# Performance work log

Hardware: AMD Instinct MI355X
Metric: run time of the kernel (lower is better)

Reference implementation:

```python
import jax, jax.numpy as jnp
import numpy as np

B, L, E, C = 64, 1024, 320, 32
H = int(E * 1.5)  # hidden_dim = 480
LAYER_NUM = 7
EPS = 1e-5


def setup_inputs() -> dict:
    key = jax.random.key(0)
    ks = jax.random.split(key, 12)
    rn = lambda k, shape: jax.random.normal(k, shape, jnp.float32) * 0.02
    return {
        "x": jax.random.normal(ks[0], (B, L, E), jnp.float32),
        "snr": jnp.array([10.0], jnp.float32),
        # final LayerNorm params
        "norm_w": jnp.ones((E,), jnp.float32),
        "norm_b": jnp.zeros((E,), jnp.float32),
        "sm0_w": rn(ks[1], (H, E)), "sm0_b": jnp.zeros((H,), jnp.float32),
        "sm_mid_w": rn(ks[2], (LAYER_NUM - 1, H, H)), "sm_mid_b": jnp.zeros((LAYER_NUM - 1, H), jnp.float32),
        "sm_last_w": rn(ks[3], (E, H)), "sm_last_b": jnp.zeros((E,), jnp.float32),
        # bm_list: 7 AdaptiveModulators, each Linear(1,H)->ReLU->Linear(H,H)->ReLU->Linear(H,H)->Sigmoid
        "bm_w1": rn(ks[4], (LAYER_NUM, H, 1)), "bm_b1": jnp.zeros((LAYER_NUM, H), jnp.float32),
        "bm_w2": rn(ks[5], (LAYER_NUM, H, H)), "bm_b2": jnp.zeros((LAYER_NUM, H), jnp.float32),
        "bm_w3": rn(ks[6], (LAYER_NUM, H, H)), "bm_b3": jnp.zeros((LAYER_NUM, H), jnp.float32),
        # head_list: Linear(E, C)
        "head_w": rn(ks[7], (C, E)), "head_b": jnp.zeros((C,), jnp.float32),
    }


def reference(x, snr, norm_w, norm_b, sm0_w, sm0_b, sm_mid_w, sm_mid_b,
              sm_last_w, sm_last_b, bm_w1, bm_b1, bm_w2, bm_b2, bm_w3, bm_b3,
              head_w, head_b):
    # Final encoder LayerNorm (torch default: biased var, eps=1e-5)
    mu = jnp.mean(x, axis=-1, keepdims=True)
    var = jnp.var(x, axis=-1, keepdims=True)
    xn = (x - mu) / jnp.sqrt(var + EPS) * norm_w + norm_b  # (B, L, E)

    b = x.shape[0]
    snr_batch = jnp.broadcast_to(snr.reshape(1, -1), (b, 1))  # (B, 1)

    # SA modulation chain (x is detached for the modulator input)
    temp = jax.lax.stop_gradient(xn) @ sm0_w.T + sm0_b  # (B, L, H)
    for i in range(LAYER_NUM):
        if i > 0:
            temp = temp @ sm_mid_w[i - 1].T + sm_mid_b[i - 1]
        h = jax.nn.relu(snr_batch @ bm_w1[i].T + bm_b1[i])      # (B, H)
        h = jax.nn.relu(h @ bm_w2[i].T + bm_b2[i])
        bm = jax.nn.sigmoid(h @ bm_w3[i].T + bm_b3[i])          # (B, H)
        temp = temp * bm[:, None, :]

    mod_val = jax.nn.sigmoid(temp @ sm_last_w.T + sm_last_b)    # (B, L, E)
    xg = xn * mod_val
    return xg @ head_w.T + head_b                               # (B, L, C)
```

## Files before the change

kernel.cpp:

```cpp
#include <hip/hip_runtime.h>

#define E_ 320
#define C_ 32
#define H_ 480
#define NL 7
#define EPS_ 1e-5f

typedef unsigned short u16;
typedef __attribute__((ext_vector_type(8))) short short8;
typedef __attribute__((ext_vector_type(4))) float f32x4;

__device__ __forceinline__ float bsf(u16 u) { return __uint_as_float(((unsigned)u) << 16); }
__device__ __forceinline__ u16 f2b(float f) {
    unsigned u = __float_as_uint(f);
    return (u16)((u + 0x7FFFu + ((u >> 16) & 1u)) >> 16);
}
__device__ __forceinline__ bool snr_is_f32(const void* snr) { return ((const u16*)snr)[0] == 0; }
__device__ __forceinline__ float ldv(const void* p, long i, bool f32) {
    return f32 ? ((const float*)p)[i] : bsf(((const u16*)p)[i]);
}

__device__ __forceinline__ u16* xsp(u16* xs, int r, int cb) {
    return (u16*)((char*)xs + (r * 640 + (cb ^ ((r & 7) << 4))));
}

__device__ __forceinline__ void load_split8(const void* W, long idx, bool f32,
                                            float g, short8& whi, short8& wlo)
{
    float wf[8];
    if (f32) {
        const float4 w0 = *(const float4*)((const float*)W + idx);
        const float4 w1 = *(const float4*)((const float*)W + idx + 4);
        wf[0]=w0.x; wf[1]=w0.y; wf[2]=w0.z; wf[3]=w0.w;
        wf[4]=w1.x; wf[5]=w1.y; wf[6]=w1.z; wf[7]=w1.w;
    } else {
        const ushort4 u0 = *(const ushort4*)((const u16*)W + idx);
        const ushort4 u1 = *(const ushort4*)((const u16*)W + idx + 4);
        wf[0]=bsf(u0.x); wf[1]=bsf(u0.y); wf[2]=bsf(u0.z); wf[3]=bsf(u0.w);
        wf[4]=bsf(u1.x); wf[5]=bsf(u1.y); wf[6]=bsf(u1.z); wf[7]=bsf(u1.w);
    }
#pragma unroll
    for (int j = 0; j < 8; ++j) {
        const float v = wf[j] * g;
        const u16 h = f2b(v);
        whi[j] = (short)h;
        wlo[j] = (short)f2b(v - bsf(h));
    }
}

__global__ void k_h2pack(const void* __restrict__ w1, const void* __restrict__ b1,
                         const void* __restrict__ w2, const void* __restrict__ b2,
                         const void* __restrict__ snr, float* __restrict__ h2out,
                         const void* __restrict__ hw, u16* __restrict__ Hb)
{
    const bool f32 = snr_is_f32(snr);
    const int bid = blockIdx.x, tid = threadIdx.x;
    if (bid >= 840) {
        const int idx = (bid - 840) * 256 + tid;
        const int cc = idx / E_, e = idx - cc * E_;
        const float v = ldv(hw, (long)cc * E_ + e, f32);
        const long o = ((long)((cc >> 4) * 10 + (e >> 5)) * 64
                        + ((e >> 3) & 3) * 16 + (cc & 15)) * 8 + (e & 7);
        Hb[o] = f2b(v);
        return;
    }
    const int i = bid / 120;
    const int lane = tid & 63, wv = tid >> 6;
    __shared__ float h1[H_];
    const float s = ldv(snr, 0, f32);
    for (int k = tid; k < H_; k += 256)
        h1[k] = fmaxf(0.f, ldv(w1, (long)i * H_ + k, f32) * s + ldv(b1, (long)i * H_ + k, f32));
    __syncthreads();
    const int n = (bid % 120) * 4 + wv;
    const long base = (long)i * H_ * H_ + (long)n * H_;
    float p = 0.f;
#pragma unroll
    for (int ks = 0; ks < 8; ++ks) {
        const int k = lane + ks * 64;
        if (k < H_) p += ldv(w2, base + k, f32) * h1[k];
    }
#pragma unroll
    for (int o = 1; o < 64; o <<= 1) p += __shfl_xor(p, o, 64);
    if (lane == 0)
        h2out[(long)i * H_ + n] = fmaxf(0.f, p + ldv(b2, (long)i * H_ + n, f32));
}

__global__ void k_s3(const void* __restrict__ w3, const void* __restrict__ b3,
                     const void* __restrict__ snr,
                     const float* __restrict__ h2in, float* __restrict__ bmout)
{
    const bool f32 = snr_is_f32(snr);
    const int i = blockIdx.x, tid = threadIdx.x;
    const int lane = tid & 63, wv = tid >> 6;
    __shared__ float h2[H_];
    for (int k = tid; k < H_; k += 256) h2[k] = h2in[(long)i * H_ + k];
    __syncthreads();
    const int n = blockIdx.y * 4 + wv;
    const long base = (long)i * H_ * H_ + (long)n * H_;
    float p = 0.f;
#pragma unroll
    for (int ks = 0; ks < 8; ++ks) {
        const int k = lane + ks * 64;
        if (k < H_) p += ldv(w3, base + k, f32) * h2[k];
    }
#pragma unroll
    for (int o = 1; o < 64; o <<= 1) p += __shfl_xor(p, o, 64);
    if (lane == 0)
        bmout[(long)i * H_ + n] = 1.f / (1.f + __expf(-(p + ldv(b3, (long)i * H_ + n, f32))));
}

__global__ __launch_bounds__(256) void k_lvl1(
    const void* __restrict__ sm0_w, const void* __restrict__ sm0_b,
    const void* __restrict__ smw, const void* __restrict__ smb,
    const void* __restrict__ slw, const void* __restrict__ slb,
    const void* __restrict__ snr, const float* __restrict__ bm,
    u16* __restrict__ N1hi, u16* __restrict__ N1lo,
    u16* __restrict__ N2Thi, u16* __restrict__ N2Tlo, float* __restrict__ bias2,
    u16* __restrict__ N3hi, u16* __restrict__ N3lo,
    u16* __restrict__ N4Thi, u16* __restrict__ N4Tlo, float* __restrict__ bias4)
{
    const bool f32 = snr_is_f32(snr);
    __shared__ u16 AH[16 * 488];
    __shared__ u16 AL[16 * 488];
    const int tid = threadIdx.x, lane = tid & 63, wv = tid >> 6;
    const int bid = blockIdx.x;

    int nodeId, bl;
    if      (bid < 168) { nodeId = 0; bl = bid; }
    else if (bid < 416) { nodeId = 1; bl = bid - 168; }
    else if (bid < 664) { nodeId = 2; bl = bid - 416; }
    else                { nodeId = 3; bl = bid - 664; }

    const void *Wa, *ba, *Wb, *bb;
    long waO, baO, wbO, bbO;
    int Sa, Adim, Nt, ntg, mode, Arows;
    const float *ga, *gb;
    u16 *Ohi, *Olo; float* bOut;
    switch (nodeId) {
    case 0:
        Wa = sm0_w; waO = 0; Sa = E_; ba = sm0_b; baO = 0; ga = bm;
        Wb = smw; wbO = 0; bb = smb; bbO = 0; gb = bm + H_;
        Adim = E_; Arows = 321; Nt = 30; ntg = 8; mode = 0;
        Ohi = N1hi; Olo = N1lo; bOut = nullptr; break;
    case 1:
        Wa = smw; waO = 1L * H_ * H_; Sa = H_; ba = smb; baO = 1L * H_; ga = bm + 2 * H_;
        Wb = smw; wbO = 2L * H_ * H_; bb = smb; bbO = 2L * H_; gb = bm + 3 * H_;
        Adim = H_; Arows = 481; Nt = 30; ntg = 8; mode = 1;
        Ohi = N2Thi; Olo = N2Tlo; bOut = bias2; break;
    case 2:
        Wa = smw; waO = 3L * H_ * H_; Sa = H_; ba = smb; baO = 3L * H_; ga = bm + 4 * H_;
        Wb = smw; wbO = 4L * H_ * H_; bb = smb; bbO = 4L * H_; gb = bm + 5 * H_;
        Adim = H_; Arows = 481; Nt = 30; ntg = 8; mode = 0;
        Ohi = N3hi; Olo = N3lo; bOut = nullptr; break;
    default:
        Wa = smw; waO = 5L * H_ * H_; Sa = H_; ba = smb; baO = 5L * H_; ga = bm + 6 * H_;
        Wb = slw; wbO = 0; bb = slb; bbO = 0; gb = nullptr;
        Adim = H_; Arows = 481; Nt = 20; ntg = 5; mode = 1;
        Ohi = N4Thi; Olo = N4Tlo; bOut = bias4; break;
    }
    const int mt = bl / ntg, ng = bl % ntg;

    for (int p = 0; p < 30; ++p) {
        const int k = p * 16 + (tid >> 4), mm = tid & 15;
        const int mg = mt * 16 + mm;
        float v;
        if (mg < Adim)       v = ldv(Wa, waO + (long)k * Sa + mg, f32);
        else if (mg == Adim) v = ldv(ba, baO + k, f32);
        else                 v = 0.f;
        v *= ga[k];
        const u16 h = f2b(v);
        AH[mm * 488 + k] = h;
        AL[mm * 488 + k] = f2b(v - bsf(h));
    }
    __syncthreads();

    const int nt = ng * 4 + wv;
    if (nt >= Nt) return;
    const int m15 = lane & 15, q2 = lane >> 4;
    const int n = nt * 16 + m15;
    const float gbn = gb ? gb[n] : 1.f;
    const u16* ahp = &AH[m15 * 488 + q2 * 8];
    const u16* alp = &AL[m15 * 488 + q2 * 8];
    const long wrow = wbO + (long)n * H_ + q2 * 8;
    f32x4 acc = {0.f, 0.f, 0.f, 0.f};
    for (int k0 = 0; k0 < H_; k0 += 32) {
        const short8 a_hi = *(const short8*)(ahp + k0);
        const short8 a_lo = *(const short8*)(alp + k0);
        short8 whi, wlo;
        load_split8(Wb, wrow + k0, f32, gbn, whi, wlo);
        acc = __builtin_amdgcn_mfma_f32_16x16x32_bf16(a_hi, whi, acc, 0, 0, 0);
        acc = __builtin_amdgcn_mfma_f32_16x16x32_bf16(a_lo, whi, acc, 0, 0, 0);
        acc = __builtin_amdgcn_mfma_f32_16x16x32_bf16(a_hi, wlo, acc, 0, 0, 0);
    }
    const float bbn = ldv(bb, bbO + n, f32) * gbn;
#pragma unroll
    for (int r = 0; r < 4; ++r) {
        const int m = mt * 16 + q2 * 4 + r;
        float v = acc[r];
        if (m == Adim) v += bbn;
        if (mode == 0) {
            if (m >= Arows) v = 0.f;
            const u16 hi = f2b(v);
            Ohi[(long)m * H_ + n] = hi;
            Olo[(long)m * H_ + n] = f2b(v - bsf(hi));
        } else {
            if (m < Adim) {
                const u16 hi = f2b(v);
                Ohi[(long)n * H_ + m] = hi;
                Olo[(long)n * H_ + m] = f2b(v - bsf(hi));
            } else if (m == Adim) {
                bOut[n] = v;
            }
        }
    }
}

__global__ __launch_bounds__(64) void k_pair(
    const u16* __restrict__ Ahi, const u16* __restrict__ Alo,
    const u16* __restrict__ Bhi, const u16* __restrict__ Blo,
    const float* __restrict__ biasB,
    u16* __restrict__ Ohi, u16* __restrict__ Olo, float* __restrict__ bOut,
    u16* __restrict__ Mb, float* __restrict__ c_row,
    int Ntn, int Adim, int Arows, int mode)
{
    const int bid = blockIdx.x;
    const int mt = bid / Ntn, nt = bid % Ntn;
    const int lane = threadIdx.x;
    const int m15 = lane & 15, q2 = lane >> 4;
    const u16* ah = Ahi + (long)(mt * 16 + m15) * H_ + q2 * 8;
    const u16* al = Alo + (long)(mt * 16 + m15) * H_ + q2 * 8;
    const u16* bh = Bhi + (long)(nt * 16 + m15) * H_ + q2 * 8;
    const u16* bl = Blo + (long)(nt * 16 + m15) * H_ + q2 * 8;
    f32x4 acc = {0.f, 0.f, 0.f, 0.f};
    for (int k0 = 0; k0 < H_; k0 += 32) {
        const short8 a_hi = *(const short8*)(ah + k0);
        const short8 a_lo = *(const short8*)(al + k0);
        const short8 b_hi = *(const short8*)(bh + k0);
        const short8 b_lo = *(const short8*)(bl + k0);
        acc = __builtin_amdgcn_mfma_f32_16x16x32_bf16(a_hi, b_hi, acc, 0, 0, 0);
        acc = __builtin_amdgcn_mfma_f32_16x16x32_bf16(a_lo, b_hi, acc, 0, 0, 0);
        acc = __builtin_amdgcn_mfma_f32_16x16x32_bf16(a_hi, b_lo, acc, 0, 0, 0);
    }
    const int n = nt * 16 + m15;
    const float bB = biasB[n];
#pragma unroll
    for (int r = 0; r < 4; ++r) {
        const int m = mt * 16 + q2 * 4 + r;
        float v = acc[r];
        if (m == Adim) v += bB;
        if (mode == 0) {
            if (m >= Arows) v = 0.f;
            const u16 hi = f2b(v);
            Ohi[(long)m * H_ + n] = hi;
            Olo[(long)m * H_ + n] = f2b(v - bsf(hi));
        } else if (mode == 1) {
            if (m < Adim) {
                const u16 hi = f2b(v);
                Ohi[(long)n * H_ + m] = hi;
                Olo[(long)n * H_ + m] = f2b(v - bsf(hi));
            } else if (m == Adim) {
                bOut[n] = v;
            }
        } else {
            if (m < E_) {
                const long idx = ((long)((n >> 4) * 10 + (m >> 5)) * 64
                                  + ((m >> 3) & 3) * 16 + (n & 15)) * 8 + (m & 7);
                Mb[idx] = f2b(v);
            } else if (m == E_) {
                c_row[n] = v;
            }
        }
    }
}

__global__ __launch_bounds__(256, 4) void main_kernel(
    const void* __restrict__ x, const void* __restrict__ nw, const void* __restrict__ nb,
    const u16* __restrict__ Mb, const float* __restrict__ c_row,
    const u16* __restrict__ Hb, const void* __restrict__ hb,
    const void* __restrict__ snr, void* __restrict__ out)
{
    const bool f32 = snr_is_f32(snr);
    __shared__ __align__(16) u16 xs[64 * 320];
    const int tid = threadIdx.x;
    const int lane = tid & 63;
    const int wv = tid >> 6;
    const long tok0 = (long)blockIdx.x * 64;

    float nwv[8], nbv[8];
#pragma unroll
    for (int i = 0; i < 4; ++i) {
        nwv[i] = ldv(nw, lane * 4 + i, f32);
        nbv[i] = ldv(nb, lane * 4 + i, f32);
    }
    if (lane < 16) {
#pragma unroll
        for (int i = 0; i < 4; ++i) {
            nwv[4 + i] = ldv(nw, 256 + lane * 4 + i, f32);
            nbv[4 + i] = ldv(nb, 256 + lane * 4 + i, f32);
        }
    }

    for (int t = 0; t < 16; ++t) {
        const int tok = wv * 16 + t;
        const long xb = (tok0 + tok) * E_;
        float v[8];
        if (f32) {
            const float4 p = *(const float4*)((const float*)x + xb + lane * 4);
            v[0] = p.x; v[1] = p.y; v[2] = p.z; v[3] = p.w;
            if (lane < 16) {
                const float4 p2 = *(const float4*)((const float*)x + xb + 256 + lane * 4);
                v[4] = p2.x; v[5] = p2.y; v[6] = p2.z; v[7] = p2.w;
            } else { v[4] = v[5] = v[6] = v[7] = 0.f; }
        } else {
            const ushort4 p = *(const ushort4*)((const u16*)x + xb + lane * 4);
            v[0] = bsf(p.x); v[1] = bsf(p.y); v[2] = bsf(p.z); v[3] = bsf(p.w);
            if (lane < 16) {
                const ushort4 p2 = *(const ushort4*)((const u16*)x + xb + 256 + lane * 4);
                v[4] = bsf(p2.x); v[5] = bsf(p2.y); v[6] = bsf(p2.z); v[7] = bsf(p2.w);
            } else { v[4] = v[5] = v[6] = v[7] = 0.f; }
        }
        float s = 0.f, ss = 0.f;
#pragma unroll
        for (int i = 0; i < 8; ++i) { s += v[i]; ss += v[i] * v[i]; }
#pragma unroll
        for (int o = 1; o < 64; o <<= 1) {
            s  += __shfl_xor(s, o, 64);
            ss += __shfl_xor(ss, o, 64);
        }
        const float mu = s * (1.f / E_);
        const float var = ss * (1.f / E_) - mu * mu;
        const float rstd = rsqrtf(var + EPS_);
        ushort4 w;
        w.x = f2b((v[0] - mu) * rstd * nwv[0] + nbv[0]);
        w.y = f2b((v[1] - mu) * rstd * nwv[1] + nbv[1]);
        w.z = f2b((v[2] - mu) * rstd * nwv[2] + nbv[2]);
        w.w = f2b((v[3] - mu) * rstd * nwv[3] + nbv[3]);
        *(ushort4*)xsp(xs, tok, lane * 8) = w;
        if (lane < 16) {
            ushort4 w2;
            w2.x = f2b((v[4] - mu) * rstd * nwv[4] + nbv[4]);
            w2.y = f2b((v[5] - mu) * rstd * nwv[5] + nbv[5]);
            w2.z = f2b((v[6] - mu) * rstd * nwv[6] + nbv[6]);
            w2.w = f2b((v[7] - mu) * rstd * nwv[7] + nbv[7]);
            *(ushort4*)xsp(xs, tok, 512 + lane * 8) = w2;
        }
    }
    __syncthreads();

    const int m15 = lane & 15, q2 = lane >> 4;
    f32x4 acc[4][5];
#pragma unroll
    for (int at = 0; at < 4; ++at)
#pragma unroll
        for (int nt = 0; nt < 5; ++nt) acc[at][nt] = (f32x4){0.f, 0.f, 0.f, 0.f};

    for (int kt = 0; kt < 10; ++kt) {
        short8 a[4];
#pragma unroll
        for (int at = 0; at < 4; ++at)
            a[at] = *(const short8*)xsp(xs, at * 16 + m15, kt * 64 + q2 * 16);
#pragma unroll
        for (int nt = 0; nt < 5; ++nt) {
            const short8 b = *(const short8*)&Mb[(((wv * 5 + nt) * 10 + kt) << 9) + (lane << 3)];
#pragma unroll
            for (int at = 0; at < 4; ++at)
                acc[at][nt] = __builtin_amdgcn_mfma_f32_16x16x32_bf16(a[at], b, acc[at][nt], 0, 0, 0);
        }
    }
    float cadd[5];
#pragma unroll
    for (int nt = 0; nt < 5; ++nt) cadd[nt] = c_row[(wv * 5 + nt) * 16 + m15];

    __syncthreads();

#pragma unroll
    for (int at = 0; at < 4; ++at)
#pragma unroll
        for (int nt = 0; nt < 5; ++nt)
#pragma unroll
            for (int r = 0; r < 4; ++r) {
                const int tok = at * 16 + q2 * 4 + r;
                const int ep = (wv * 5 + nt) * 16 + m15;
                const float z = acc[at][nt][r] + cadd[nt];
                const float mod = 1.f / (1.f + __expf(-z));
                u16* cell = xsp(xs, tok, ep * 2);
                *cell = f2b(bsf(*cell) * mod);
            }
    __syncthreads();

    const int ct = wv & 1, ab = (wv >> 1) * 2;
    f32x4 oa[2];
    oa[0] = (f32x4){0.f, 0.f, 0.f, 0.f};
    oa[1] = (f32x4){0.f, 0.f, 0.f, 0.f};
    for (int kt = 0; kt < 10; ++kt) {
        const short8 a0 = *(const short8*)xsp(xs, (ab + 0) * 16 + m15, kt * 64 + q2 * 16);
        const short8 a1 = *(const short8*)xsp(xs, (ab + 1) * 16 + m15, kt * 64 + q2 * 16);
        const short8 b = *(const short8*)&Hb[((ct * 10 + kt) << 9) + (lane << 3)];
        oa[0] = __builtin_amdgcn_mfma_f32_16x16x32_bf16(a0, b, oa[0], 0, 0, 0);
        oa[1] = __builtin_amdgcn_mfma_f32_16x16x32_bf16(a1, b, oa[1], 0, 0, 0);
    }
    const float hbv = ldv(hb, ct * 16 + m15, f32);
#pragma unroll
    for (int i2 = 0; i2 < 2; ++i2)
#pragma unroll
        for (int r = 0; r < 4; ++r) {
            const long tok = tok0 + (ab + i2) * 16 + q2 * 4 + r;
            const float v = oa[i2][r] + hbv;
            const long o = tok * C_ + ct * 16 + m15;
            if (f32) ((float*)out)[o] = v;
            else     ((u16*)out)[o] = f2b(v);
        }
}

extern "C" void kernel_launch(void* const* d_in, const int* in_sizes, int n_in,
                              void* d_out, int out_size, void* d_ws, size_t ws_size,
                              hipStream_t stream)
{
    (void)in_sizes; (void)n_in; (void)out_size; (void)ws_size;
    const void* x         = d_in[0];
    const void* snr       = d_in[1];
    const void* norm_w    = d_in[2];
    const void* norm_b    = d_in[3];
    const void* sm0_w     = d_in[4];
    const void* sm0_b     = d_in[5];
    const void* sm_mid_w  = d_in[6];
    const void* sm_mid_b  = d_in[7];
    const void* sm_last_w = d_in[8];
    const void* sm_last_b = d_in[9];
    const void* bm_w1     = d_in[10];
    const void* bm_b1     = d_in[11];
    const void* bm_w2     = d_in[12];
    const void* bm_b2     = d_in[13];
    const void* bm_w3     = d_in[14];
    const void* bm_b3     = d_in[15];
    const void* head_w    = d_in[16];
    const void* head_b    = d_in[17];

    char* ws = (char*)d_ws;
    u16*   Mb    = (u16*)(ws);
    float* c_row = (float*)(ws + 204800);
    u16*   Hb    = (u16*)(ws + 206080);
    float* h2    = (float*)(ws + 226560);
    float* bm    = (float*)(ws + 240000);

    char* ob = (char*)d_out;
    u16* N1hi  = (u16*)(ob + 0);
    u16* N1lo  = (u16*)(ob + 322560);
    u16* N2Thi = (u16*)(ob + 645120);
    u16* N2Tlo = (u16*)(ob + 1105920);
    float* bias2 = (float*)(ob + 1566720);
    u16* N3hi  = (u16*)(ob + 1568640);
    u16* N3lo  = (u16*)(ob + 2044800);
    u16* N4Thi = (u16*)(ob + 2520960);
    u16* N4Tlo = (u16*)(ob + 2828160);
    float* bias4 = (float*)(ob + 3135360);
    u16* N5hi  = (u16*)(ob + 3136640);
    u16* N5lo  = (u16*)(ob + 3459200);
    u16* N6Thi = (u16*)(ob + 0);
    u16* N6Tlo = (u16*)(ob + 307200);
    float* bias6 = (float*)(ob + 614400);

    k_h2pack<<<880, 256, 0, stream>>>(bm_w1, bm_b1, bm_w2, bm_b2, snr, h2, head_w, Hb);
    k_s3<<<dim3(NL, 120), 256, 0, stream>>>(bm_w3, bm_b3, snr, h2, bm);
    k_lvl1<<<819, 256, 0, stream>>>(sm0_w, sm0_b, sm_mid_w, sm_mid_b,
                                    sm_last_w, sm_last_b, snr, bm,
                                    N1hi, N1lo, N2Thi, N2Tlo, bias2,
                                    N3hi, N3lo, N4Thi, N4Tlo, bias4);
    k_pair<<<630, 64, 0, stream>>>(N1hi, N1lo, N2Thi, N2Tlo, bias2,
                                   N5hi, N5lo, nullptr, nullptr, nullptr,
                                   30, E_, 321, 0);
    k_pair<<<620, 64, 0, stream>>>(N3hi, N3lo, N4Thi, N4Tlo, bias4,
                                   N6Thi, N6Tlo, bias6, nullptr, nullptr,
                                   20, H_, 481, 1);
    k_pair<<<420, 64, 0, stream>>>(N5hi, N5lo, N6Thi, N6Tlo, bias6,
                                   nullptr, nullptr, nullptr, Mb, c_row,
                                   20, E_, 321, 2);
    main_kernel<<<1024, 256, 0, stream>>>(x, norm_w, norm_b, Mb, c_row, Hb, head_b, snr, d_out);
}
```

Before: 261.4 us.

## Fuse modulator MLP kernels and vectorize gate epilogue with packed bf16 converts

Merges the two small modulator kernels into one 68-block kernel in which each block recomputes the full hidden layer h2 for its layer into shared memory and then computes a quarter of the sigmoid outputs. This removes one launch and the global round trip for h2, at the cost of four-fold redundant work on the second matvec and far fewer blocks. In the main kernel, the MFMA operands are swapped so each lane holds four consecutive features of one token. That lets the sigmoid gating epilogue do vectorized 8-byte LDS read-modify-writes, and it uses the hardware packed bf16 conversion instruction in place of scalar software rounding.

```diff
diff --git a/kernel.cpp b/kernel.cpp
--- a/kernel.cpp
+++ b/kernel.cpp
@@ -14,6 +14,11 @@
 __device__ __forceinline__ u16 f2b(float f) {
     unsigned u = __float_as_uint(f);
     return (u16)((u + 0x7FFFu + ((u >> 16) & 1u)) >> 16);
+}
+__device__ __forceinline__ unsigned f2b_pk(float a, float b) {
+    unsigned r;
+    asm("v_cvt_pk_bf16_f32 %0, %1, %2" : "=v"(r) : "v"(a), "v"(b));
+    return r;
 }
 __device__ __forceinline__ bool snr_is_f32(const void* snr) { return ((const u16*)snr)[0] == 0; }
 __device__ __forceinline__ float ldv(const void* p, long i, bool f32) {
@@ -48,15 +53,17 @@
     }
 }
 
-__global__ void k_h2pack(const void* __restrict__ w1, const void* __restrict__ b1,
-                         const void* __restrict__ w2, const void* __restrict__ b2,
-                         const void* __restrict__ snr, float* __restrict__ h2out,
-                         const void* __restrict__ hw, u16* __restrict__ Hb)
+__global__ __launch_bounds__(256) void k_bm(
+    const void* __restrict__ w1, const void* __restrict__ b1,
+    const void* __restrict__ w2, const void* __restrict__ b2,
+    const void* __restrict__ w3, const void* __restrict__ b3,
+    const void* __restrict__ snr, const void* __restrict__ hw,
+    u16* __restrict__ Hb, float* __restrict__ bmout)
 {
     const bool f32 = snr_is_f32(snr);
     const int bid = blockIdx.x, tid = threadIdx.x;
-    if (bid >= 840) {
-        const int idx = (bid - 840) * 256 + tid;
+    if (bid >= 28) {
+        const int idx = (bid - 28) * 256 + tid;
         const int cc = idx / E_, e = idx - cc * E_;
         const float v = ldv(hw, (long)cc * E_ + e, f32);
         const long o = ((long)((cc >> 4) * 10 + (e >> 5)) * 64
@@ -64,49 +71,42 @@
         Hb[o] = f2b(v);
         return;
     }
-    const int i = bid / 120;
+    const int i = bid >> 2, g = bid & 3;
     const int lane = tid & 63, wv = tid >> 6;
     __shared__ float h1[H_];
+    __shared__ float h2s[H_];
     const float s = ldv(snr, 0, f32);
     for (int k = tid; k < H_; k += 256)
         h1[k] = fmaxf(0.f, ldv(w1, (long)i * H_ + k, f32) * s + ldv(b1, (long)i * H_ + k, f32));
     __syncthreads();
-    const int n = (bid % 120) * 4 + wv;
-    const long base = (long)i * H_ * H_ + (long)n * H_;
-    float p = 0.f;
-#pragma unroll
-    for (int ks = 0; ks < 8; ++ks) {
-        const int k = lane + ks * 64;
-        if (k < H_) p += ldv(w2, base + k, f32) * h1[k];
-    }
-#pragma unroll
-    for (int o = 1; o < 64; o <<= 1) p += __shfl_xor(p, o, 64);
-    if (lane == 0)
-        h2out[(long)i * H_ + n] = fmaxf(0.f, p + ldv(b2, (long)i * H_ + n, f32));
-}
-
-__global__ void k_s3(const void* __restrict__ w3, const void* __restrict__ b3,
-                     const void* __restrict__ snr,
-                     const float* __restrict__ h2in, float* __restrict__ bmout)
-{
-    const bool f32 = snr_is_f32(snr);
-    const int i = blockIdx.x, tid = threadIdx.x;
-    const int lane = tid & 63, wv = tid >> 6;
-    __shared__ float h2[H_];
-    for (int k = tid; k < H_; k += 256) h2[k] = h2in[(long)i * H_ + k];
-    __syncthreads();
-    const int n = blockIdx.y * 4 + wv;
-    const long base = (long)i * H_ * H_ + (long)n * H_;
-    float p = 0.f;
-#pragma unroll
-    for (int ks = 0; ks < 8; ++ks) {
-        const int k = lane + ks * 64;
-        if (k < H_) p += ldv(w3, base + k, f32) * h2[k];
-    }
-#pragma unroll
-    for (int o = 1; o < 64; o <<= 1) p += __shfl_xor(p, o, 64);
-    if (lane == 0)
-        bmout[(long)i * H_ + n] = 1.f / (1.f + __expf(-(p + ldv(b3, (long)i * H_ + n, f32))));
+    for (int n = wv; n < H_; n += 4) {
+        const long base = (long)i * H_ * H_ + (long)n * H_;
+        float p = 0.f;
+#pragma unroll
+        for (int ks = 0; ks < 8; ++ks) {
+            const int k = lane + ks * 64;
+            if (k < H_) p += ldv(w2, base + k, f32) * h1[k];
+        }
+#pragma unroll
+        for (int o = 1; o < 64; o <<= 1) p += __shfl_xor(p, o, 64);
+        if (lane == 0)
+            h2s[n] = fmaxf(0.f, p + ldv(b2, (long)i * H_ + n, f32));
+    }
+    __syncthreads();
+    for (int n0 = wv; n0 < 120; n0 += 4) {
+        const int n = g * 120 + n0;
+        const long base = (long)i * H_ * H_ + (long)n * H_;
+        float p = 0.f;
+#pragma unroll
+        for (int ks = 0; ks < 8; ++ks) {
+            const int k = lane + ks * 64;
+            if (k < H_) p += ldv(w3, base + k, f32) * h2s[k];
+        }
+#pragma unroll
+        for (int o = 1; o < 64; o <<= 1) p += __shfl_xor(p, o, 64);
+        if (lane == 0)
+            bmout[(long)i * H_ + n] = 1.f / (1.f + __expf(-(p + ldv(b3, (long)i * H_ + n, f32))));
+    }
 }
 
 __global__ __launch_bounds__(256) void k_lvl1(
@@ -330,19 +330,19 @@
         const float mu = s * (1.f / E_);
         const float var = ss * (1.f / E_) - mu * mu;
         const float rstd = rsqrtf(var + EPS_);
-        ushort4 w;
-        w.x = f2b((v[0] - mu) * rstd * nwv[0] + nbv[0]);
-        w.y = f2b((v[1] - mu) * rstd * nwv[1] + nbv[1]);
-        w.z = f2b((v[2] - mu) * rstd * nwv[2] + nbv[2]);
-        w.w = f2b((v[3] - mu) * rstd * nwv[3] + nbv[3]);
-        *(ushort4*)xsp(xs, tok, lane * 8) = w;
+        uint2 w;
+        w.x = f2b_pk((v[0] - mu) * rstd * nwv[0] + nbv[0],
+                     (v[1] - mu) * rstd * nwv[1] + nbv[1]);
+        w.y = f2b_pk((v[2] - mu) * rstd * nwv[2] + nbv[2],
+                     (v[3] - mu) * rstd * nwv[3] + nbv[3]);
+        *(uint2*)xsp(xs, tok, lane * 8) = w;
         if (lane < 16) {
-            ushort4 w2;
-            w2.x = f2b((v[4] - mu) * rstd * nwv[4] + nbv[4]);
-            w2.y = f2b((v[5] - mu) * rstd * nwv[5] + nbv[5]);
-            w2.z = f2b((v[6] - mu) * rstd * nwv[6] + nbv[6]);
-            w2.w = f2b((v[7] - mu) * rstd * nwv[7] + nbv[7]);
-            *(ushort4*)xsp(xs, tok, 512 + lane * 8) = w2;
+            uint2 w2;
+            w2.x = f2b_pk((v[4] - mu) * rstd * nwv[4] + nbv[4],
+                          (v[5] - mu) * rstd * nwv[5] + nbv[5]);
+            w2.y = f2b_pk((v[6] - mu) * rstd * nwv[6] + nbv[6],
+                          (v[7] - mu) * rstd * nwv[7] + nbv[7]);
+            *(uint2*)xsp(xs, tok, 512 + lane * 8) = w2;
         }
     }
     __syncthreads();
@@ -364,28 +364,38 @@
             const short8 b = *(const short8*)&Mb[(((wv * 5 + nt) * 10 + kt) << 9) + (lane << 3)];
 #pragma unroll
             for (int at = 0; at < 4; ++at)
-                acc[at][nt] = __builtin_amdgcn_mfma_f32_16x16x32_bf16(a[at], b, acc[at][nt], 0, 0, 0);
-        }
-    }
-    float cadd[5];
-#pragma unroll
-    for (int nt = 0; nt < 5; ++nt) cadd[nt] = c_row[(wv * 5 + nt) * 16 + m15];
-
-    __syncthreads();
-
-#pragma unroll
-    for (int at = 0; at < 4; ++at)
-#pragma unroll
-        for (int nt = 0; nt < 5; ++nt)
-#pragma unroll
-            for (int r = 0; r < 4; ++r) {
-                const int tok = at * 16 + q2 * 4 + r;
-                const int ep = (wv * 5 + nt) * 16 + m15;
-                const float z = acc[at][nt][r] + cadd[nt];
-                const float mod = 1.f / (1.f + __expf(-z));
-                u16* cell = xsp(xs, tok, ep * 2);
-                *cell = f2b(bsf(*cell) * mod);
-            }
+                acc[at][nt] = __builtin_amdgcn_mfma_f32_16x16x32_bf16(b, a[at], acc[at][nt], 0, 0, 0);
+        }
+    }
+    float4 cadd4[5];
+#pragma unroll
+    for (int nt = 0; nt < 5; ++nt)
+        cadd4[nt] = *(const float4*)&c_row[(wv * 5 + nt) * 16 + q2 * 4];
+
+    __syncthreads();
+
+#pragma unroll
+    for (int at = 0; at < 4; ++at) {
+        const int tok = at * 16 + m15;
+#pragma unroll
+        for (int nt = 0; nt < 5; ++nt) {
+            const int e0 = (wv * 5 + nt) * 16 + q2 * 4;
+            uint2* cell = (uint2*)xsp(xs, tok, e0 * 2);
+            uint2 u = *cell;
+            const float4 ca = cadd4[nt];
+            const float z0 = acc[at][nt][0] + ca.x;
+            const float z1 = acc[at][nt][1] + ca.y;
+            const float z2 = acc[at][nt][2] + ca.z;
+            const float z3 = acc[at][nt][3] + ca.w;
+            const float g0 = bsf((u16)(u.x & 0xffff)) / (1.f + __expf(-z0));
+            const float g1 = bsf((u16)(u.x >> 16))    / (1.f + __expf(-z1));
+            const float g2 = bsf((u16)(u.y & 0xffff)) / (1.f + __expf(-z2));
+            const float g3 = bsf((u16)(u.y >> 16))    / (1.f + __expf(-z3));
+            u.x = f2b_pk(g0, g1);
+            u.y = f2b_pk(g2, g3);
+            *cell = u;
+        }
+    }
     __syncthreads();
 
     const int ct = wv & 1, ab = (wv >> 1) * 2;
@@ -440,8 +450,7 @@
     u16*   Mb    = (u16*)(ws);
     float* c_row = (float*)(ws + 204800);
     u16*   Hb    = (u16*)(ws + 206080);
-    float* h2    = (float*)(ws + 226560);
-    float* bm    = (float*)(ws + 240000);
+    float* bm    = (float*)(ws + 226560);
 
     char* ob = (char*)d_out;
     u16* N1hi  = (u16*)(ob + 0);
@@ -460,8 +469,8 @@
     u16* N6Tlo = (u16*)(ob + 307200);
     float* bias6 = (float*)(ob + 614400);
 
-    k_h2pack<<<880, 256, 0, stream>>>(bm_w1, bm_b1, bm_w2, bm_b2, snr, h2, head_w, Hb);
-    k_s3<<<dim3(NL, 120), 256, 0, stream>>>(bm_w3, bm_b3, snr, h2, bm);
+    k_bm<<<68, 256, 0, stream>>>(bm_w1, bm_b1, bm_w2, bm_b2, bm_w3, bm_b3,
+                                 snr, head_w, Hb, bm);
     k_lvl1<<<819, 256, 0, stream>>>(sm0_w, sm0_b, sm_mid_w, sm_mid_b,
                                     sm_last_w, sm_last_b, snr, bm,
                                     N1hi, N1lo, N2Thi, N2Tlo, bias2,
```

After: 480.5 us. 1.84x slower.
